# Optimization experiments

Hardware: AMD Instinct MI355X
Metric: run time of the kernel (lower is better)

Reference implementation:

```python
import jax, jax.numpy as jnp
import numpy as np

B, C, H, W = 256, 1024, 14, 14
C8 = C // 8
TXT = 150 * 1024  # flattened text embed dim
N = H * W  # 196, matches self.l shape (1,196)


def setup_inputs() -> dict:
    key = jax.random.key(0)
    ks = jax.random.split(key, 12)
    s = lambda fan_in: 1.0 / np.sqrt(fan_in)
    return {
        "x": jax.random.normal(ks[0], (B, C, H, W), jnp.float32),
        "text_embed": jax.random.normal(ks[1], (B, 1, 150, 1024), jnp.float32),
        "G_w": jax.random.normal(ks[2], (C, TXT), jnp.float32) * s(TXT),
        "G_b": jnp.zeros((C,), jnp.float32),
        "l": jax.random.normal(ks[3], (1, N), jnp.float32) * 0.02,
        "W_q": jax.random.normal(ks[4], (C8, C), jnp.float32) * s(C),
        "b_q": jnp.zeros((C8,), jnp.float32),
        "W_k": jax.random.normal(ks[5], (C8, C), jnp.float32) * s(C),
        "b_k": jnp.zeros((C8,), jnp.float32),
        "W_v": jax.random.normal(ks[6], (C, C), jnp.float32) * s(C),
        "b_v": jnp.zeros((C,), jnp.float32),
        "gamma": jnp.ones((1,), jnp.float32) * 0.5,
    }


def reference(x, text_embed, G_w, G_b, l, W_q, b_q, W_k, b_k, W_v, b_v, gamma):
    b, c, h, w = x.shape
    n = h * w
    # text preprocessing: squeeze(1) + flatten + Linear G -> (B, C)
    te = text_embed.reshape(b, -1) @ G_w.T + G_b  # (B, C)
    # bmm(te[:, :, None], l broadcast) == outer product per batch -> (B, C, N)
    te_flat = te[:, :, None] * l[None, 0, None, :]  # (B, C, N)
    x_flat = x.reshape(b, c, n)  # (B, C, N)
    # 1x1 convs == channel matmuls
    proj_query = jnp.einsum('qc,bcn->bnq', W_q, x_flat) + b_q  # (B, N, C8)
    proj_key = jnp.einsum('kc,bcn->bkn', W_k, te_flat) + b_k[None, :, None]  # (B, C8, N)
    energy = jnp.einsum('bnq,bqm->bnm', proj_query, proj_key)  # (B, N, N)
    attention = jax.nn.softmax(energy, axis=-1)  # (B, N, N)
    proj_value = jnp.einsum('vc,bcn->bvn', W_v, te_flat) + b_v[None, :, None]  # (B, C, N)
    # out = bmm(value, attention^T): out[b,c,m] = sum_n value[b,c,n] * attn[b,m,n]
    out = jnp.einsum('bcn,bmn->bcm', proj_value, attention)  # (B, C, N)
    out = out.reshape(b, c, h, w)
    return gamma * out + x
```

## Files before the change

### kernel.cpp

```cpp
#include <hip/hip_runtime.h>
#include <hip/hip_bf16.h>

#define BB 256
#define CC 1024
#define CQ 128
#define NN 196
#define TXTK 153600
#define SPLITS 64
#define KCHUNK 2400
#define KSTEPS 75
#define LDP 40

typedef __attribute__((ext_vector_type(8))) short short8;
typedef __attribute__((ext_vector_type(4))) float f32x4;
typedef __attribute__((ext_vector_type(2))) unsigned int u32x2;

static __device__ __forceinline__ unsigned int pkbf(float a, float b) {
  __hip_bfloat162 t = __float22bfloat162_rn(make_float2(a, b));
  unsigned int r;
  __builtin_memcpy(&r, &t, 4);
  return r;
}

static __device__ __forceinline__ float bflo(unsigned int u) {
  unsigned int v = u << 16;
  float f;
  __builtin_memcpy(&f, &v, 4);
  return f;
}
static __device__ __forceinline__ float bfhi(unsigned int u) {
  unsigned int v = u & 0xffff0000u;
  float f;
  __builtin_memcpy(&f, &v, 4);
  return f;
}

__global__ __launch_bounds__(1024) void k1_gemm_partial(
    const float* __restrict__ TE, const float* __restrict__ Gw,
    unsigned int* __restrict__ part) {
  __shared__ unsigned short Al[2][256 * LDP];
  __shared__ unsigned short Bl[2][256 * LDP];

  const int tid = threadIdx.x;
  const int fid = blockIdx.x;
  const int r8 = fid & 7;
  const int nt = (fid >> 3) & 3;
  const int sp = (fid >> 5) * 8 + r8;
  const int kbase = sp * KCHUNK;

  const int lane = tid & 63;
  const int w = tid >> 6;
  const int wm = w & 3;
  const int wn = w >> 2;

  const int r0 = tid >> 3;
  const int c0 = (tid & 7) * 4;
  const float* Ap0 = TE + (size_t)r0 * TXTK + kbase + c0;
  const float* Ap1 = TE + (size_t)(r0 + 128) * TXTK + kbase + c0;
  const float* Bp0 = Gw + (size_t)(nt * 256 + r0) * TXTK + kbase + c0;
  const float* Bp1 = Gw + (size_t)(nt * 256 + r0 + 128) * TXTK + kbase + c0;
  const int l0 = r0 * LDP + c0;
  const int l1 = (r0 + 128) * LDP + c0;

  f32x4 ra0, ra1, rb0, rb1;
  auto loadRegs = [&](int ko) {
    ra0 = *(const f32x4*)(Ap0 + ko);
    ra1 = *(const f32x4*)(Ap1 + ko);
    rb0 = __builtin_nontemporal_load((const f32x4*)(Bp0 + ko));
    rb1 = __builtin_nontemporal_load((const f32x4*)(Bp1 + ko));
  };
  auto cvt4 = [](f32x4 v) {
    uint2 h;
    h.x = pkbf(v.x, v.y);
    h.y = pkbf(v.z, v.w);
    return h;
  };
  auto writeLDS = [&](int buf) {
    *(uint2*)&Al[buf][l0] = cvt4(ra0);
    *(uint2*)&Al[buf][l1] = cvt4(ra1);
    *(uint2*)&Bl[buf][l0] = cvt4(rb0);
    *(uint2*)&Bl[buf][l1] = cvt4(rb1);
  };

  f32x4 acc[4][4];
  const f32x4 z = {0.f, 0.f, 0.f, 0.f};
#pragma unroll
  for (int i = 0; i < 4; ++i)
#pragma unroll
    for (int j = 0; j < 4; ++j) acc[i][j] = z;

  loadRegs(0);
  writeLDS(0);
  __syncthreads();

  const int k8 = (lane >> 4) * 8;
  const int fr = lane & 15;

  for (int ks = 0; ks < KSTEPS; ++ks) {
    const int cur = ks & 1;
    if (ks + 1 < KSTEPS) loadRegs((ks + 1) * 32);

    short8 bfr[4];
#pragma unroll
    for (int ns = 0; ns < 4; ++ns) {
      int col = wn * 64 + ns * 16 + fr;
      bfr[ns] = *(const short8*)&Bl[cur][col * LDP + k8];
    }
#pragma unroll
    for (int ms = 0; ms < 4; ++ms) {
      int row = wm * 64 + ms * 16 + fr;
      short8 af = *(const short8*)&Al[cur][row * LDP + k8];
#pragma unroll
      for (int ns = 0; ns < 4; ++ns)
        acc[ms][ns] = __builtin_amdgcn_mfma_f32_16x16x32_bf16(af, bfr[ns], acc[ms][ns], 0, 0, 0);
    }

    if (ks + 1 < KSTEPS) writeLDS(cur ^ 1);
    __syncthreads();
  }

  u32x2* d2 = (u32x2*)part + (size_t)(sp * 4 + nt) * 16384;
#pragma unroll
  for (int ms = 0; ms < 4; ++ms)
#pragma unroll
    for (int ns = 0; ns < 4; ++ns) {
      u32x2 pk;
      pk.x = pkbf(acc[ms][ns][0], acc[ms][ns][1]);
      pk.y = pkbf(acc[ms][ns][2], acc[ms][ns][3]);
      const int v = ms * 4 + ns;
      __builtin_nontemporal_store(pk, d2 + v * 1024 + tid);
    }
}

__global__ __launch_bounds__(1024) void k2_reduce(
    const unsigned int* __restrict__ part, const float* __restrict__ Gb,
    float* __restrict__ te) {
  const int idx = blockIdx.x * 1024 + threadIdx.x;
  const int nt = idx >> 14;
  const int s = idx & 16383;
  const u32x2* p2 = (const u32x2*)part;

  float a0 = 0.f, a1 = 0.f, a2 = 0.f, a3 = 0.f;
#pragma unroll 4
  for (int sp = 0; sp < SPLITS; ++sp) {
    u32x2 u = p2[(size_t)(sp * 4 + nt) * 16384 + s];
    a0 += bflo(u.x); a1 += bfhi(u.x);
    a2 += bflo(u.y); a3 += bfhi(u.y);
  }

  const int v = s >> 10, t = s & 1023;
  const int lane = t & 63, w = t >> 6;
  const int wm = w & 3, wn = w >> 2;
  const int ms = v >> 2, ns = v & 3;
  const int b0 = wm * 64 + ms * 16 + (lane >> 4) * 4;
  const int c = nt * 256 + wn * 64 + ns * 16 + (lane & 15);
  const float gb = Gb[c];
  te[(size_t)(b0 + 0) * CC + c] = a0 + gb;
  te[(size_t)(b0 + 1) * CC + c] = a1 + gb;
  te[(size_t)(b0 + 2) * CC + c] = a2 + gb;
  te[(size_t)(b0 + 3) * CC + c] = a3 + gb;
}

__global__ __launch_bounds__(256) void k3_dual(
    const float* __restrict__ te, const float* __restrict__ Wk,
    const float* __restrict__ Wv, float* __restrict__ kbuf,
    float* __restrict__ vbuf) {
  __shared__ float As[64][33];
  __shared__ float Bs[64][33];
  const int tid = threadIdx.x;
  const int tx = tid & 15, ty = tid >> 4;
  const int bx = blockIdx.x;
  const float* Wt;
  float* outp;
  int Nout, n0;
  if (bx < 2) { Wt = Wk; outp = kbuf; Nout = CQ; n0 = bx * 64; }
  else        { Wt = Wv; outp = vbuf; Nout = CC; n0 = (bx - 2) * 64; }
  const int m0 = blockIdx.y * 64;
  float acc[4][4] = {};
  for (int k0 = 0; k0 < CC; k0 += 32) {
#pragma unroll
    for (int j = 0; j < 2; ++j) {
      int i = tid + 256 * j;
      int r = i >> 3, c4 = (i & 7) * 4;
      f32x4 va = *(const f32x4*)(te + (size_t)(m0 + r) * CC + k0 + c4);
      As[r][c4 + 0] = va.x; As[r][c4 + 1] = va.y; As[r][c4 + 2] = va.z; As[r][c4 + 3] = va.w;
      f32x4 vb4 = *(const f32x4*)(Wt + (size_t)(n0 + r) * CC + k0 + c4);
      Bs[r][c4 + 0] = vb4.x; Bs[r][c4 + 1] = vb4.y; Bs[r][c4 + 2] = vb4.z; Bs[r][c4 + 3] = vb4.w;
    }
    __syncthreads();
#pragma unroll 8
    for (int k = 0; k < 32; ++k) {
      float a[4], bv[4];
#pragma unroll
      for (int i = 0; i < 4; ++i) a[i] = As[ty * 4 + i][k];
#pragma unroll
      for (int j = 0; j < 4; ++j) bv[j] = Bs[tx * 4 + j][k];
#pragma unroll
      for (int i = 0; i < 4; ++i)
#pragma unroll
        for (int j = 0; j < 4; ++j) acc[i][j] += a[i] * bv[j];
    }
    __syncthreads();
  }
#pragma unroll
  for (int i = 0; i < 4; ++i)
#pragma unroll
    for (int j = 0; j < 4; ++j)
      outp[(size_t)(m0 + ty * 4 + i) * Nout + n0 + tx * 4 + j] = acc[i][j];
}

__global__ __launch_bounds__(1024) void k4a_attn(
    const float* __restrict__ x, const float* __restrict__ kb,
    const float* __restrict__ Wq, const float* __restrict__ bq,
    float* __restrict__ pbuf) {
  __shared__ float kbs[CQ];
  __shared__ float wqs[512];
  __shared__ float partl[16][NN];
  __shared__ float dsh;

  const int h = blockIdx.x;
  const int b = blockIdx.y;
  const int ch0 = h * 512;
  const int tid = threadIdx.x;

  if (tid < CQ) kbs[tid] = kb[b * CQ + tid];
  __syncthreads();

  if (tid < 512) {
    float s = 0.f;
#pragma unroll 8
    for (int q = 0; q < CQ; ++q) s += Wq[q * CC + ch0 + tid] * kbs[q];
    wqs[tid] = s;
  }
  if (tid == 1023) {
    float d = 0.f;
    if (h == 0)
      for (int q = 0; q < CQ; ++q) d += bq[q] * kbs[q];
    dsh = d;
  }
  __syncthreads();

  const float* xb = x + (size_t)b * (CC * NN) + (size_t)ch0 * NN;
  if (tid < 784) {
    const int r = tid / 49, n4 = tid % 49;
    f32x4 acc = {0.f, 0.f, 0.f, 0.f};
#pragma unroll 4
    for (int c = r; c < 512; c += 16) {
      f32x4 v = *(const f32x4*)(xb + c * NN + n4 * 4);
      acc += wqs[c] * v;
    }
    partl[r][n4 * 4 + 0] = acc.x;
    partl[r][n4 * 4 + 1] = acc.y;
    partl[r][n4 * 4 + 2] = acc.z;
    partl[r][n4 * 4 + 3] = acc.w;
  }
  __syncthreads();
  if (tid < NN) {
    float s = dsh;
#pragma unroll
    for (int r = 0; r < 16; ++r) s += partl[r][tid];
    pbuf[b * 400 + h * 200 + tid] = s;
  }
}

__global__ __launch_bounds__(256) void k4mid(
    const float* __restrict__ pbuf, const float* __restrict__ l,
    float* __restrict__ sbuf) {
  __shared__ float ls[NN];
  __shared__ float av[NN];
  const int b = blockIdx.x;
  const int tid = threadIdx.x;
  if (tid < NN) {
    ls[tid] = l[tid];
    av[tid] = pbuf[b * 400 + tid] + pbuf[b * 400 + 200 + tid];
  }
  __syncthreads();
  if (tid < NN) {
    const float a = av[tid];
    float m = -1e30f;
    for (int j = 0; j < NN; ++j) m = fmaxf(m, a * ls[j]);
    float num = 0.f, den = 0.f;
    for (int j = 0; j < NN; ++j) {
      float e = __expf(a * ls[j] - m);
      num += ls[j] * e;
      den += e;
    }
    sbuf[b * NN + tid] = num / den;
  }
}

__global__ __launch_bounds__(256) void k4b_epilogue(
    const float* __restrict__ x, const float* __restrict__ vbuf,
    const float* __restrict__ bv, const float* __restrict__ sbuf,
    const float* __restrict__ gammap, float* __restrict__ out) {
  __shared__ __align__(16) float sv[NN];
  __shared__ float Ac[128];
  __shared__ float Bc[128];
  const int sl = blockIdx.x;
  const int b = blockIdx.y;
  const int tid = threadIdx.x;
  const float g = gammap[0];

  if (tid < NN) sv[tid] = sbuf[b * NN + tid];
  if (tid < 128) {
    Ac[tid] = g * vbuf[b * CC + sl * 128 + tid];
    Bc[tid] = g * bv[sl * 128 + tid];
  }
  __syncthreads();

  const float* xb = x + (size_t)b * (CC * NN) + (size_t)sl * 128 * NN;
  float* ob = out + (size_t)b * (CC * NN) + (size_t)sl * 128 * NN;
  for (int f = tid; f < 6272; f += 256) {
    const int c = f / 49;
    const int n4 = f - c * 49;
    f32x4 xv = *(const f32x4*)(xb + f * 4);
    f32x4 s4 = *(const f32x4*)&sv[n4 * 4];
    f32x4 o = Ac[c] * s4 + (Bc[c] + xv);
    __builtin_nontemporal_store(o, (f32x4*)(ob + f * 4));
  }
}

extern "C" void kernel_launch(void* const* d_in, const int* in_sizes, int n_in,
                              void* d_out, int out_size, void* d_ws, size_t ws_size,
                              hipStream_t stream) {
  const float* x    = (const float*)d_in[0];
  const float* TE   = (const float*)d_in[1];
  const float* Gw   = (const float*)d_in[2];
  const float* Gb   = (const float*)d_in[3];
  const float* l    = (const float*)d_in[4];
  const float* Wq   = (const float*)d_in[5];
  const float* bq   = (const float*)d_in[6];
  const float* Wk   = (const float*)d_in[7];
  const float* Wv   = (const float*)d_in[9];
  const float* bv   = (const float*)d_in[10];
  const float* gam  = (const float*)d_in[11];

  float* out  = (float*)d_out;
  unsigned int* part = (unsigned int*)d_out;
  float* pbuf = out + 20000000;
  float* te   = (float*)d_ws;
  float* kbuf = te + BB * CC;
  float* vbuf = kbuf + BB * CQ;
  float* sbuf = vbuf + BB * CC;

  hipLaunchKernelGGL(k1_gemm_partial, dim3(256), dim3(1024), 0, stream, TE, Gw, part);
  hipLaunchKernelGGL(k2_reduce, dim3(64), dim3(1024), 0, stream, part, Gb, te);
  hipLaunchKernelGGL(k3_dual, dim3(18, 4), dim3(256), 0, stream, te, Wk, Wv, kbuf, vbuf);
  hipLaunchKernelGGL(k4a_attn, dim3(2, BB), dim3(1024), 0, stream, x, kbuf, Wq, bq, pbuf);
  hipLaunchKernelGGL(k4mid, dim3(BB), dim3(256), 0, stream, pbuf, l, sbuf);
  hipLaunchKernelGGL(k4b_epilogue, dim3(8, BB), dim3(256), 0, stream, x, vbuf, bv, sbuf, gam, out);
}
```

Baseline: 388.7 us.

## Widen split-K GEMM K-tile to 64 with half-step pipelining and fewer splits

The split-K text-projection GEMM now works on 64-wide K steps over 60 splits instead of 32-wide steps over 64. Each thread loads 8 contiguous floats per row, and the next tile's loads and LDS writes are interleaved between the two MFMA halves. This cuts the number of barriers and partial results and gives wider global loads. The reduce kernel now uses nontemporal loads, the epilogue walks batches in reverse (likely for cache reuse of recently written data), and pbuf moves into the workspace. Costs: more LDS per block, and 16 of the 256 launched blocks exit early.

```diff
diff --git a/kernel.cpp b/kernel.cpp
--- a/kernel.cpp
+++ b/kernel.cpp
@@ -6,10 +6,10 @@
 #define CQ 128
 #define NN 196
 #define TXTK 153600
-#define SPLITS 64
-#define KCHUNK 2400
-#define KSTEPS 75
-#define LDP 40
+#define SPLITS 60
+#define KCHUNK 2560
+#define KSTEPS 40
+#define LDP 68
 
 typedef __attribute__((ext_vector_type(8))) short short8;
 typedef __attribute__((ext_vector_type(4))) float f32x4;
@@ -44,8 +44,11 @@
   const int tid = threadIdx.x;
   const int fid = blockIdx.x;
   const int r8 = fid & 7;
-  const int nt = (fid >> 3) & 3;
-  const int sp = (fid >> 5) * 8 + r8;
+  const int idx = fid >> 3;
+  const int nt = idx & 3;
+  const int z = idx >> 2;
+  const int sp = z * 8 + r8;
+  if (sp >= SPLITS) return;
   const int kbase = sp * KCHUNK;
 
   const int lane = tid & 63;
@@ -53,69 +56,81 @@
   const int wm = w & 3;
   const int wn = w >> 2;
 
-  const int r0 = tid >> 3;
-  const int c0 = (tid & 7) * 4;
-  const float* Ap0 = TE + (size_t)r0 * TXTK + kbase + c0;
-  const float* Ap1 = TE + (size_t)(r0 + 128) * TXTK + kbase + c0;
-  const float* Bp0 = Gw + (size_t)(nt * 256 + r0) * TXTK + kbase + c0;
-  const float* Bp1 = Gw + (size_t)(nt * 256 + r0 + 128) * TXTK + kbase + c0;
-  const int l0 = r0 * LDP + c0;
-  const int l1 = (r0 + 128) * LDP + c0;
-
-  f32x4 ra0, ra1, rb0, rb1;
-  auto loadRegs = [&](int ko) {
-    ra0 = *(const f32x4*)(Ap0 + ko);
-    ra1 = *(const f32x4*)(Ap1 + ko);
-    rb0 = __builtin_nontemporal_load((const f32x4*)(Bp0 + ko));
-    rb1 = __builtin_nontemporal_load((const f32x4*)(Bp1 + ko));
+  const int r = tid >> 2;
+  const int cq = (tid & 3) * 8;
+  const float* Ap = TE + (size_t)r * TXTK + kbase + cq;
+  const float* Bp = Gw + (size_t)(nt * 256 + r) * TXTK + kbase + cq;
+  const int lws = r * LDP + cq;
+
+  f32x4 a0, a1, b0, b1;
+  auto loadHalf = [&](int ko) {
+    a0 = *(const f32x4*)(Ap + ko);
+    a1 = *(const f32x4*)(Ap + ko + 4);
+    b0 = __builtin_nontemporal_load((const f32x4*)(Bp + ko));
+    b1 = __builtin_nontemporal_load((const f32x4*)(Bp + ko + 4));
   };
-  auto cvt4 = [](f32x4 v) {
-    uint2 h;
-    h.x = pkbf(v.x, v.y);
-    h.y = pkbf(v.z, v.w);
-    return h;
+  auto writeHalf = [&](int buf, int off) {
+    uint4 ha, hb;
+    ha.x = pkbf(a0.x, a0.y); ha.y = pkbf(a0.z, a0.w);
+    ha.z = pkbf(a1.x, a1.y); ha.w = pkbf(a1.z, a1.w);
+    hb.x = pkbf(b0.x, b0.y); hb.y = pkbf(b0.z, b0.w);
+    hb.z = pkbf(b1.x, b1.y); hb.w = pkbf(b1.z, b1.w);
+    *(uint4*)&Al[buf][lws + off] = ha;
+    *(uint4*)&Bl[buf][lws + off] = hb;
   };
-  auto writeLDS = [&](int buf) {
-    *(uint2*)&Al[buf][l0] = cvt4(ra0);
-    *(uint2*)&Al[buf][l1] = cvt4(ra1);
-    *(uint2*)&Bl[buf][l0] = cvt4(rb0);
-    *(uint2*)&Bl[buf][l1] = cvt4(rb1);
-  };
 
   f32x4 acc[4][4];
-  const f32x4 z = {0.f, 0.f, 0.f, 0.f};
+  const f32x4 z4 = {0.f, 0.f, 0.f, 0.f};
 #pragma unroll
   for (int i = 0; i < 4; ++i)
 #pragma unroll
-    for (int j = 0; j < 4; ++j) acc[i][j] = z;
-
-  loadRegs(0);
-  writeLDS(0);
-  __syncthreads();
-
-  const int k8 = (lane >> 4) * 8;
+    for (int j = 0; j < 4; ++j) acc[i][j] = z4;
+
+  loadHalf(0);
+  writeHalf(0, 0);
+  loadHalf(32);
+  writeHalf(0, 32);
+  __syncthreads();
+
   const int fr = lane & 15;
+  const int kb8 = (lane >> 4) * 8;
 
   for (int ks = 0; ks < KSTEPS; ++ks) {
     const int cur = ks & 1;
-    if (ks + 1 < KSTEPS) loadRegs((ks + 1) * 32);
-
-    short8 bfr[4];
-#pragma unroll
-    for (int ns = 0; ns < 4; ++ns) {
-      int col = wn * 64 + ns * 16 + fr;
-      bfr[ns] = *(const short8*)&Bl[cur][col * LDP + k8];
-    }
-#pragma unroll
-    for (int ms = 0; ms < 4; ++ms) {
-      int row = wm * 64 + ms * 16 + fr;
-      short8 af = *(const short8*)&Al[cur][row * LDP + k8];
+    const bool pre = (ks + 1 < KSTEPS);
+    if (pre) loadHalf((ks + 1) * 64);
+
+    {
+      short8 bfr[4];
 #pragma unroll
       for (int ns = 0; ns < 4; ++ns)
-        acc[ms][ns] = __builtin_amdgcn_mfma_f32_16x16x32_bf16(af, bfr[ns], acc[ms][ns], 0, 0, 0);
-    }
-
-    if (ks + 1 < KSTEPS) writeLDS(cur ^ 1);
+        bfr[ns] = *(const short8*)&Bl[cur][(wn * 64 + ns * 16 + fr) * LDP + kb8];
+#pragma unroll
+      for (int ms = 0; ms < 4; ++ms) {
+        short8 af = *(const short8*)&Al[cur][(wm * 64 + ms * 16 + fr) * LDP + kb8];
+#pragma unroll
+        for (int ns = 0; ns < 4; ++ns)
+          acc[ms][ns] = __builtin_amdgcn_mfma_f32_16x16x32_bf16(af, bfr[ns], acc[ms][ns], 0, 0, 0);
+      }
+    }
+    if (pre) {
+      writeHalf(cur ^ 1, 0);
+      loadHalf((ks + 1) * 64 + 32);
+    }
+    {
+      short8 bfr[4];
+#pragma unroll
+      for (int ns = 0; ns < 4; ++ns)
+        bfr[ns] = *(const short8*)&Bl[cur][(wn * 64 + ns * 16 + fr) * LDP + 32 + kb8];
+#pragma unroll
+      for (int ms = 0; ms < 4; ++ms) {
+        short8 af = *(const short8*)&Al[cur][(wm * 64 + ms * 16 + fr) * LDP + 32 + kb8];
+#pragma unroll
+        for (int ns = 0; ns < 4; ++ns)
+          acc[ms][ns] = __builtin_amdgcn_mfma_f32_16x16x32_bf16(af, bfr[ns], acc[ms][ns], 0, 0, 0);
+      }
+    }
+    if (pre) writeHalf(cur ^ 1, 32);
     __syncthreads();
   }
 
@@ -143,7 +158,7 @@
   float a0 = 0.f, a1 = 0.f, a2 = 0.f, a3 = 0.f;
 #pragma unroll 4
   for (int sp = 0; sp < SPLITS; ++sp) {
-    u32x2 u = p2[(size_t)(sp * 4 + nt) * 16384 + s];
+    u32x2 u = __builtin_nontemporal_load(p2 + (size_t)(sp * 4 + nt) * 16384 + s);
     a0 += bflo(u.x); a1 += bfhi(u.x);
     a2 += bflo(u.y); a3 += bfhi(u.y);
   }
@@ -297,7 +312,7 @@
   __shared__ float Ac[128];
   __shared__ float Bc[128];
   const int sl = blockIdx.x;
-  const int b = blockIdx.y;
+  const int b = 255 - blockIdx.y;
   const int tid = threadIdx.x;
   const float g = gammap[0];
 
@@ -337,11 +352,11 @@
 
   float* out  = (float*)d_out;
   unsigned int* part = (unsigned int*)d_out;
-  float* pbuf = out + 20000000;
   float* te   = (float*)d_ws;
   float* kbuf = te + BB * CC;
   float* vbuf = kbuf + BB * CQ;
   float* sbuf = vbuf + BB * CC;
+  float* pbuf = sbuf + BB * NN;
 
   hipLaunchKernelGGL(k1_gemm_partial, dim3(256), dim3(1024), 0, stream, TE, Gw, part);
   hipLaunchKernelGGL(k2_reduce, dim3(64), dim3(1024), 0, stream, part, Gb, te);
```

New measurement: 436.3 us. +12.2%, slower.
